# Performance work log

Hardware: AMD Instinct MI355X
Metric: run time of the kernel (lower is better)

Reference implementation:

```python
import jax, jax.numpy as jnp
from jax import lax
import numpy as np

B, N, C = 4, 2000, 80           # images, proposals/img, foreground classes
SCORE_THR = 0.05
IOU_THR = 0.5
MAX_PER_IMG = 100
K_PRE = 2000                     # pre-NMS top-k candidates per image
STDS = np.array([0.1, 0.1, 0.2, 0.2], dtype=np.float32)
MAX_RATIO = float(abs(np.log(16.0 / 1000.0)))  # wh_ratio_clip=16/1000


def setup_inputs() -> dict:
    key = jax.random.key(0)
    k1, k2, k3 = jax.random.split(key, 3)
    class_outs = jax.random.normal(k1, (B, N, C + 1), dtype=jnp.float32)
    regression_outs = jax.random.normal(k2, (B, N, C * 4), dtype=jnp.float32) * 0.5
    # random valid proposal boxes inside 800x1333 images (x1<x2, y1<y2)
    xy = jax.random.uniform(k3, (B, N, 2, 2), dtype=jnp.float32)
    xy = xy * jnp.array([1333.0, 800.0], dtype=jnp.float32)
    lo = jnp.min(xy, axis=2)
    hi = jnp.max(xy, axis=2) + 1.0
    boxes = jnp.concatenate([lo, hi], axis=-1)  # [B,N,4] x1,y1,x2,y2
    images_hw = jnp.tile(jnp.array([[800, 1333]], dtype=jnp.int32), (B, 1))
    return {"class_outs": class_outs, "regression_outs": regression_outs,
            "boxes": boxes, "images_hw": images_hw}


def _decode(props, deltas, h, w):
    # props [N,4], deltas [N,C,4] -> decoded boxes [N,C,4], clipped to image
    d = deltas * jnp.asarray(STDS)
    dx, dy, dw, dh = d[..., 0], d[..., 1], d[..., 2], d[..., 3]
    dw = jnp.clip(dw, -MAX_RATIO, MAX_RATIO)
    dh = jnp.clip(dh, -MAX_RATIO, MAX_RATIO)
    px = (props[:, None, 0] + props[:, None, 2]) * 0.5
    py = (props[:, None, 1] + props[:, None, 3]) * 0.5
    pw = props[:, None, 2] - props[:, None, 0]
    ph = props[:, None, 3] - props[:, None, 1]
    gx = px + pw * dx
    gy = py + ph * dy
    gw = pw * jnp.exp(dw)
    gh = ph * jnp.exp(dh)
    x1 = jnp.clip(gx - gw * 0.5, 0.0, w)
    y1 = jnp.clip(gy - gh * 0.5, 0.0, h)
    x2 = jnp.clip(gx + gw * 0.5, 0.0, w)
    y2 = jnp.clip(gy + gh * 0.5, 0.0, h)
    return jnp.stack([x1, y1, x2, y2], axis=-1)


def _pairwise_iou(b):
    # b [K,4] -> iou [K,K]
    area = (b[:, 2] - b[:, 0]) * (b[:, 3] - b[:, 1])
    lt = jnp.maximum(b[:, None, :2], b[None, :, :2])
    rb = jnp.minimum(b[:, None, 2:], b[None, :, 2:])
    wh = jnp.clip(rb - lt, 0.0)
    inter = wh[..., 0] * wh[..., 1]
    return inter / (area[:, None] + area[None, :] - inter + 1e-6)


def _process_image(cls_out, reg_out, props, hw):
    h = hw[0].astype(jnp.float32)
    w = hw[1].astype(jnp.float32)
    scores = jax.nn.softmax(cls_out, axis=-1)[:, :C]          # drop background col
    bboxes = _decode(props, reg_out.reshape(N, C, 4), h, w)   # [N,C,4]
    flat_scores = scores.reshape(-1)                          # [N*C]
    flat_boxes = bboxes.reshape(-1, 4)
    labels = jnp.tile(jnp.arange(C, dtype=jnp.int32), N)      # class fastest-varying
    cand = jnp.where(flat_scores > SCORE_THR, flat_scores, -1.0)
    top_scores, top_idx = lax.top_k(cand, K_PRE)
    top_boxes = flat_boxes[top_idx]
    top_labels = labels[top_idx]
    valid = top_scores > SCORE_THR
    # class-offset trick: boxes of distinct classes never overlap
    off = top_labels.astype(jnp.float32)[:, None] * (jnp.maximum(h, w) + 1.0)
    iou = _pairwise_iou(top_boxes + off)                      # [K_PRE,K_PRE]
    idxs = jnp.arange(K_PRE)

    def body(i, keep):
        sup = (idxs > i) & (iou[i] > IOU_THR) & keep[i]
        return keep & ~sup

    keep = lax.fori_loop(0, K_PRE, body, valid)
    kept_scores = jnp.where(keep, top_scores, -1.0)
    det_scores, det_i = lax.top_k(kept_scores, MAX_PER_IMG)
    det_valid = det_scores > SCORE_THR
    det_boxes = jnp.where(det_valid[:, None], top_boxes[det_i], 0.0)
    det_labels = jnp.where(det_valid, top_labels[det_i], -1)
    det_scores = jnp.where(det_valid, det_scores, 0.0)
    return det_boxes, det_scores, det_labels


def reference(class_outs, regression_outs, boxes, images_hw):
    det_boxes, det_scores, det_labels = jax.vmap(_process_image)(
        class_outs, regression_outs, boxes, images_hw)
    return det_boxes, det_scores, det_labels
```

## Files before the change

kernel.cpp:

```cpp
#include <hip/hip_runtime.h>


typedef unsigned long long u64;
typedef unsigned int u32;

#define B_ 4
#define N_ 2000
#define C_ 80
#define NCLS 81
#define KPRE 2000
#define MAXDET 100
#define TARGET 256
#define NB 2312
#define NBPAD 2368
#define NG 37
#define HBASE 0xF500
#define KSHIFT 46
#define CAPA 320
#define CAPB 2048
#define NWAVE 16
#define SEGW 384
#define CAPBLK 128
#define BPI 125
#define BIGI 0x7fffffff

__device__ __forceinline__ u64 pack_key(float score, unsigned fi) {
  return ((u64)__float_as_uint(score) << 32) | (u64)(0xFFFFFFFFu - fi);
}

__device__ __forceinline__ float wred_max(float v) {
  int t;
#define STEPM(ctrl)                                                          \
  t = __builtin_amdgcn_update_dpp(__float_as_int(v), __float_as_int(v),      \
                                  (ctrl), 0xF, 0xF, false);                  \
  v = fmaxf(v, __int_as_float(t));
  STEPM(0x111) STEPM(0x112) STEPM(0x114) STEPM(0x118) STEPM(0x142) STEPM(0x143)
#undef STEPM
  return __int_as_float(__builtin_amdgcn_readlane(__float_as_int(v), 63));
}
__device__ __forceinline__ float wred_sum(float v) {
  int t;
#define STEPS(ctrl)                                                          \
  t = __builtin_amdgcn_update_dpp(0, __float_as_int(v), (ctrl), 0xF, 0xF,    \
                                  false);                                    \
  v = v + __int_as_float(t);
  STEPS(0x111) STEPS(0x112) STEPS(0x114) STEPS(0x118) STEPS(0x142) STEPS(0x143)
#undef STEPS
  return __int_as_float(__builtin_amdgcn_readlane(__float_as_int(v), 63));
}

__device__ __forceinline__ int dpp_min8(int v) {
  int t;
  t = __builtin_amdgcn_update_dpp(BIGI, v, 0x104, 0xF, 0xF, false);
  v = min(v, t);
  t = __builtin_amdgcn_update_dpp(BIGI, v, 0x102, 0xF, 0xF, false);
  v = min(v, t);
  t = __builtin_amdgcn_update_dpp(BIGI, v, 0x101, 0xF, 0xF, false);
  v = min(v, t);
  return v;
}

__device__ __forceinline__ float4 decode_one(
    u64 kk, const float* __restrict__ reg, const float* __restrict__ props,
    int b, float h, float w, float offscale) {
  const float MAXR = 4.135166556742356f;
  unsigned fi = 0xFFFFFFFFu - (u32)kk;
  int n = (int)(fi / (unsigned)C_);
  int c = (int)(fi - (unsigned)n * (unsigned)C_);
  float4 p = ((const float4*)props)[b * N_ + n];
  const float* dl = reg + ((size_t)(b * N_ + n)) * (C_ * 4) + c * 4;
  float dx = dl[0] * 0.1f;
  float dy = dl[1] * 0.1f;
  float dw = fminf(fmaxf(dl[2] * 0.2f, -MAXR), MAXR);
  float dh = fminf(fmaxf(dl[3] * 0.2f, -MAXR), MAXR);
  float px = (p.x + p.z) * 0.5f, py = (p.y + p.w) * 0.5f;
  float pw = p.z - p.x, ph = p.w - p.y;
  float gx = px + pw * dx, gy = py + ph * dy;
  float gw = pw * expf(dw), gh = ph * expf(dh);
  float off = (float)c * offscale;
  return make_float4(fminf(fmaxf(gx - gw * 0.5f, 0.0f), w) + off,
                     fminf(fmaxf(gy - gh * 0.5f, 0.0f), h) + off,
                     fminf(fmaxf(gx + gw * 0.5f, 0.0f), w) + off,
                     fminf(fmaxf(gy + gh * 0.5f, 0.0f), h) + off);
}

__global__ __launch_bounds__(1024) void cand_kernel(
    const float* __restrict__ cls, u64* __restrict__ gkeys, int* __restrict__ gcnt) {
  __shared__ int s_wc[16], s_woff[16];
  const int tid = threadIdx.x;
  const int w = tid >> 6, lane = tid & 63;
  const int blk = blockIdx.x;
  const int b = blk / BPI;
  const int n = (blk % BPI) * 16 + w;
  const float* lg = cls + (size_t)(b * N_ + n) * NCLS;
  float x0 = lg[lane];
  float x1 = (lane < 17) ? lg[64 + lane] : -3.0e38f;
  float mx = wred_max(fmaxf(x0, x1));
  float e0 = expf(x0 - mx);
  float e1 = (lane < 17) ? expf(x1 - mx) : 0.0f;
  float sum = wred_sum(e0 + e1);
  float sc0 = e0 / sum, sc1 = e1 / sum;
  bool p0 = sc0 > 0.05f;
  bool p1 = (lane < 16) && (sc1 > 0.05f);
  u64 m0 = __ballot(p0), m1 = __ballot(p1);
  int c0 = __popcll(m0);
  if (lane == 0) s_wc[w] = c0 + __popcll(m1);
  __syncthreads();
  if (tid == 0) {
    int acc = 0;
#pragma unroll
    for (int i = 0; i < 16; ++i) { s_woff[i] = acc; acc += s_wc[i]; }
    gcnt[blk] = acc;
  }
  __syncthreads();
  const int base = s_woff[w];
  const u64 lt = (1ull << lane) - 1;
  u64* gk = gkeys + (size_t)blk * CAPBLK;
  if (p0) {
    int slot = base + __popcll(m0 & lt);
    if (slot < CAPBLK) gk[slot] = pack_key(sc0, (unsigned)(n * C_ + lane));
  }
  if (p1) {
    int slot = base + c0 + __popcll(m1 & lt);
    if (slot < CAPBLK) gk[slot] = pack_key(sc1, (unsigned)(n * C_ + 64 + lane));
  }
}


__global__ __launch_bounds__(1024) void nms_kernel(
    const float* __restrict__ reg, const float* __restrict__ props,
    const int* __restrict__ hw, const u64* __restrict__ gkeys,
    const int* __restrict__ gcnt, float* __restrict__ out) {
  __shared__ u64 lds8[7952];
  char* bp = (char*)lds8;
  u64* keylist = (u64*)bp;
  u64* SS = (u64*)bp;
  u64* rb = (u64*)(bp + 8192);
  u64* U2 = (u64*)bp;
  u64* SSB = (u64*)(bp + 16384);
  u32* hist = (u32*)(bp + 49152);
  float4* bxA = (float4*)(bp + 49152);
  u64* U = (u64*)(bp + 58624);
  int* outl = (int*)(bp + 62720);
  int* misc = (int*)(bp + 63232);
  int* segc = (int*)(bp + 63296);
  int* s_coarse = (int*)(bp + 63360);

  const int b = blockIdx.x, tid = threadIdx.x;
  const int wv = tid >> 6, lane = tid & 63;

  float h = (float)hw[b * 2 + 0];
  float w = (float)hw[b * 2 + 1];
  float offscale = fmaxf(h, w) + 1.0f;

  if (tid < 16) misc[tid] = 0;
  if (tid < 64) s_coarse[tid] = 0;
  for (int i = tid; i < NBPAD; i += 1024) hist[i] = 0;
  __syncthreads();

  {
    int cnts[8];
#pragma unroll
    for (int k = 0; k < 8; k++) {
      int p = wv + 16 * k;
      cnts[k] = (p < BPI) ? gcnt[b * BPI + p] : 0;
    }
    bool ovf = false;
    int segoff = 0;
#pragma unroll
    for (int k = 0; k < 8; k++) {
      int p = wv + 16 * k;
      if (p >= BPI) break;
      int cnt = cnts[k];
      if (cnt > CAPBLK) { ovf = true; cnt = CAPBLK; }
      const u64* seg = gkeys + (size_t)(b * BPI + p) * CAPBLK;
#pragma unroll
      for (int r = 0; r < 2; r++) {
        int idx = lane + 64 * r;
        if (idx < cnt) {
          u64 key = seg[idx];
          int bi = min(max((int)(key >> KSHIFT) - HBASE, 0), NB - 1);
          atomicAdd(&hist[bi], 1u);
          int slot = segoff + idx;
          if (slot < SEGW) keylist[wv * SEGW + slot] = key;
        }
      }
      segoff += cnt;
    }
    if (segoff > SEGW) ovf = true;
    if (lane == 0) {
      segc[wv] = min(segoff, SEGW);
      if (ovf) misc[7] = 1;
    }
  }
  __syncthreads();

  for (int g2 = wv; g2 < NG; g2 += NWAVE) {
    int v = (int)hist[(g2 << 6) | lane];
#pragma unroll
    for (int o = 32; o; o >>= 1) v += __shfl_xor(v, o);
    if (lane == 0) s_coarse[g2] = v;
  }
  __syncthreads();

  if (tid < 64) {
    int v = s_coarse[lane];
#pragma unroll
    for (int off = 1; off < 64; off <<= 1) {
      int src = lane + off;
      int o = __shfl(v, src < 64 ? src : 63);
      if (src < 64) v += o;
    }
    int Mtot = __shfl(v, 0);
    u64 pm = __ballot(v >= TARGET);
    int T_A = 0, S_A;
    if (pm) {
      int gs = 63 - __builtin_clzll(pm);
      int beyond = __shfl(v, gs + 1);
      int fv = (int)hist[(gs << 6) | lane];
#pragma unroll
      for (int off = 1; off < 64; off <<= 1) {
        int src = lane + off;
        int o = __shfl(fv, src < 64 ? src : 63);
        if (src < 64) fv += o;
      }
      int cum = beyond + fv;
      u64 pm2 = __ballot(cum >= TARGET);
      int tr = 63 - __builtin_clzll(pm2);
      T_A = (gs << 6) + tr;
      S_A = __shfl(cum, tr);
    } else {
      S_A = Mtot;
    }
    u64 pmB = __ballot(v >= KPRE);
    int T_B = 0, S_B;
    if (pmB) {
      int gs = 63 - __builtin_clzll(pmB);
      int beyond = __shfl(v, gs + 1);
      int fv = (int)hist[(gs << 6) | lane];
#pragma unroll
      for (int off = 1; off < 64; off <<= 1) {
        int src = lane + off;
        int o = __shfl(fv, src < 64 ? src : 63);
        if (src < 64) fv += o;
      }
      int cum = beyond + fv;
      u64 pm2 = __ballot(cum >= KPRE);
      int tr = 63 - __builtin_clzll(pm2);
      T_B = (gs << 6) + tr;
      S_B = __shfl(cum, tr);
    } else {
      S_B = Mtot;
    }
    if (lane == 0) {
      misc[0] = T_A; misc[2] = S_A; misc[3] = Mtot;
      misc[1] = T_B; misc[8] = S_B; misc[4] = 0;
    }
  }
  __syncthreads();
  if (tid == 0 && misc[8] > CAPB)
    misc[1] = min(misc[1] + 1, NB - 1);
  __syncthreads();

  int T_A = misc[0], S_A = misc[2], Mtot = misc[3];
  bool modeB = (S_A > CAPA) || (misc[7] != 0);
  int K = 0, nkept = 0;

  if (!modeB) {
    for (int s = 0; s < NWAVE; s++) {
      int Mg = segc[s];
      bool pred = false;
      u64 key = 0;
      if (tid < Mg) {
        key = keylist[s * SEGW + tid];
        int bi = min(max((int)(key >> KSHIFT) - HBASE, 0), NB - 1);
        pred = (bi >= T_A);
      }
      u64 mk = __ballot(pred);
      if (mk) {
        int wbase = 0;
        if (lane == 0) wbase = atomicAdd(&misc[4], __popcll(mk));
        wbase = __shfl(wbase, 0);
        if (pred) {
          int pos = wbase + __popcll(mk & ((1ull << lane) - 1));
          if (pos < CAPA) U[pos] = key;
        }
      }
    }
    __syncthreads();
    int S = misc[4];
    if (S > CAPA) S = CAPA;
    if (tid == 0 && (S & 1)) U[S] = 0ULL;
    __syncthreads();
    if (tid < S) {
      u64 k1 = U[tid];
      int r1 = 0;
      const ulonglong2* Uu2 = (const ulonglong2*)U;
      int half = (S + 1) >> 1;
      for (int k = 0; k < half; k++) {
        ulonglong2 kk = Uu2[k];
        r1 += (kk.x > k1) + (kk.y > k1);
      }
      SS[r1] = k1;
    }
    __syncthreads();
    K = S;
    for (int j = tid; j < K; j += 1024)
      bxA[j] = decode_one(SS[j], reg, props, b, h, w, offscale);
    __syncthreads();

    int nwords = (S + 63) >> 6;
    int ntiles = nwords * (nwords + 1) / 2;
    for (int t = wv; t < ntiles; t += NWAVE) {
      int ti = 0, rem = t;
      while (rem >= nwords - ti) { rem -= nwords - ti; ti++; }
      int tj = ti + rem;
      int i = (ti << 6) + lane;
      float4 bi4 = bxA[i];
      float ai = (bi4.z - bi4.x) * (bi4.w - bi4.y);
      u64 bits = 0;
      int jbase = tj << 6;
      int jcount = min(64, S - jbase);
      for (int jj = 0; jj < jcount; jj++) {
        int j = jbase + jj;
        float4 bj = bxA[j];
        float aj = (bj.z - bj.x) * (bj.w - bj.y);
        float iw = fmaxf(fminf(bi4.z, bj.z) - fmaxf(bi4.x, bj.x), 0.0f);
        float ih = fmaxf(fminf(bi4.w, bj.w) - fmaxf(bi4.y, bj.y), 0.0f);
        float inter = iw * ih;
        float iou = inter / (ai + aj - inter + 1e-6f);
        if (j > i && iou > 0.5f) bits |= (1ull << jj);
      }
      if (i < S) rb[i * 8 + tj] = bits;
    }
    __syncthreads();

    if (tid < 64) {
      u64 alive = 0;
      if (lane < nwords) {
        alive = ~0ull;
        int remb = S & 63;
        if (lane == nwords - 1 && remb) alive = (1ull << remb) - 1;
      }
      int nk = 0;
      if (S > 0) {
        int i = 0;
        u64 row = (lane < nwords) ? rb[0 * 8 + lane] : 0ull;
        for (;;) {
          if (lane == 0) outl[nk] = i;
          nk++;
          if (nk >= MAXDET) break;
          if (lane == (i >> 6)) alive &= ~(1ull << (i & 63));
          u64 rowSpec = (i + 1 < S && lane < nwords) ? rb[(i + 1) * 8 + lane] : 0ull;
          u64 a2 = alive & ~row;
          alive = a2;
          int cnd = a2 ? ((lane << 6) + (int)__builtin_ctzll(a2)) : BIGI;
          int m8 = dpp_min8(cnd);
          int ni = __builtin_amdgcn_readfirstlane(m8);
          if (ni >= BIGI) break;
          row = (ni == i + 1) ? rowSpec
                              : ((lane < nwords) ? rb[ni * 8 + lane] : 0ull);
          i = ni;
        }
      }
      if (lane == 0) misc[6] = nk;
    }
    __syncthreads();
    nkept = misc[6];
    if (nkept < MAXDET && K < Mtot && K < KPRE) modeB = true;
  }

  if (modeB) {
    __syncthreads();
    if (tid == 0) misc[4] = 0;
    __syncthreads();
    int T_B = misc[1];
    for (int k = 0; k < 8; k++) {
      int p = wv + 16 * k;
      if (p >= BPI) break;
      int cnt = min(gcnt[b * BPI + p], CAPBLK);
      const u64* seg = gkeys + (size_t)(b * BPI + p) * CAPBLK;
#pragma unroll
      for (int r = 0; r < 2; r++) {
        int idx = lane + 64 * r;
        bool pred = false;
        u64 key = 0;
        if (idx < cnt) {
          key = seg[idx];
          int bi = min(max((int)(key >> KSHIFT) - HBASE, 0), NB - 1);
          pred = (bi >= T_B);
        }
        u64 mk = __ballot(pred);
        if (mk) {
          int wbase = 0;
          if (lane == 0) wbase = atomicAdd(&misc[4], __popcll(mk));
          wbase = __shfl(wbase, 0);
          if (pred) {
            int pos = wbase + __popcll(mk & ((1ull << lane) - 1));
            if (pos < CAPB) U2[pos] = key;
          }
        }
      }
    }
    __syncthreads();
    int S = misc[4];
    if (S > CAPB) S = CAPB;
    {
      int j1 = tid, j2 = tid + 1024;
      u64 k1 = (j1 < S) ? U2[j1] : 0ULL;
      u64 k2 = (j2 < S) ? U2[j2] : 0ULL;
      int r1 = 0, r2 = 0;
      for (int k = 0; k < S; k++) {
        u64 kk = U2[k];
        r1 += (kk > k1);
        r2 += (kk > k2);
      }
      __syncthreads();
      if (j1 < S) SSB[r1] = k1;
      if (j2 < S) SSB[r2] = k2;
    }
    __syncthreads();
    K = (S < KPRE) ? S : KPRE;
    int j1 = tid, j2 = tid + 1024;
    bool kp1 = (j1 < K), kp2 = (j2 < K);
    float4 bb1 = kp1 ? decode_one(SSB[j1], reg, props, b, h, w, offscale)
                     : make_float4(0, 0, 0, 0);
    float4 bb2 = kp2 ? decode_one(SSB[j2], reg, props, b, h, w, offscale)
                     : make_float4(0, 0, 0, 0);
    int nk = 0;
    if (K > 0) {
      int i = 0;
      for (;;) {
        if (tid == 0) { outl[nk] = i; misc[5] = K; }
        nk++;
        if (nk >= MAXDET) break;
        __syncthreads();
        float4 tb = decode_one(SSB[i], reg, props, b, h, w, offscale);
        float ai = (tb.z - tb.x) * (tb.w - tb.y);
        int ln = K;
        if (kp1 && j1 > i) {
          float aj = (bb1.z - bb1.x) * (bb1.w - bb1.y);
          float iw = fmaxf(fminf(tb.z, bb1.z) - fmaxf(tb.x, bb1.x), 0.0f);
          float ih = fmaxf(fminf(tb.w, bb1.w) - fmaxf(tb.y, bb1.y), 0.0f);
          float inter = iw * ih;
          float iou = inter / (ai + aj - inter + 1e-6f);
          if (iou > 0.5f) kp1 = false;
          else ln = min(ln, j1);
        }
        if (kp2 && j2 > i) {
          float aj = (bb2.z - bb2.x) * (bb2.w - bb2.y);
          float iw = fmaxf(fminf(tb.z, bb2.z) - fmaxf(tb.x, bb2.x), 0.0f);
          float ih = fmaxf(fminf(tb.w, bb2.w) - fmaxf(tb.y, bb2.y), 0.0f);
          float inter = iw * ih;
          float iou = inter / (ai + aj - inter + 1e-6f);
          if (iou > 0.5f) kp2 = false;
          else ln = min(ln, j2);
        }
#pragma unroll
        for (int off = 32; off; off >>= 1) ln = min(ln, __shfl_xor(ln, off));
        if ((tid & 63) == 0 && ln < K) atomicMin(&misc[5], ln);
        __syncthreads();
        int ni = misc[5];
        __syncthreads();
        if (ni >= K) break;
        i = ni;
      }
    }
    if (tid == 0) misc[6] = nk;
    __syncthreads();
    nkept = misc[6];
  }

  float* oBox = out;
  float* oSc = out + B_ * MAXDET * 4;
  float* oLb = out + B_ * MAXDET * 5;
  for (int k2 = tid; k2 < MAXDET; k2 += 1024) {
    float4 bb = make_float4(0.0f, 0.0f, 0.0f, 0.0f);
    float sv = 0.0f, lv = -1.0f;
    if (k2 < nkept) {
      int idx = outl[k2];
      u64 kk = modeB ? SSB[idx] : SS[idx];
      sv = __uint_as_float((u32)(kk >> 32));
      unsigned fi = 0xFFFFFFFFu - (u32)kk;
      int c = (int)(fi % (unsigned)C_);
      float off = (float)c * offscale;
      float4 ob = modeB ? decode_one(kk, reg, props, b, h, w, offscale) : bxA[idx];
      bb = make_float4(ob.x - off, ob.y - off, ob.z - off, ob.w - off);
      lv = (float)c;
    }
    oBox[(b * MAXDET + k2) * 4 + 0] = bb.x;
    oBox[(b * MAXDET + k2) * 4 + 1] = bb.y;
    oBox[(b * MAXDET + k2) * 4 + 2] = bb.z;
    oBox[(b * MAXDET + k2) * 4 + 3] = bb.w;
    oSc[b * MAXDET + k2] = sv;
    oLb[b * MAXDET + k2] = lv;
  }
}

extern "C" void kernel_launch(void* const* d_in, const int* in_sizes, int n_in,
                              void* d_out, int out_size, void* d_ws, size_t ws_size,
                              hipStream_t stream) {
  const float* cls = (const float*)d_in[0];
  const float* reg = (const float*)d_in[1];
  const float* props = (const float*)d_in[2];
  const int* hw = (const int*)d_in[3];
  float* out = (float*)d_out;

  int* gcnt = (int*)d_ws;
  u64* gkeys = (u64*)((char*)d_ws + 2048);

  cand_kernel<<<B_ * BPI, 1024, 0, stream>>>(cls, gkeys, gcnt);
  nms_kernel<<<B_, 1024, 0, stream>>>(reg, props, hw, gkeys, gcnt, out);
}
```

Baseline: 108.0 us.

## Split NMS kernel into fast-path and fallback kernels gated by flag

Splits the single NMS kernel into a fast-path kernel (mode A) and a separate fallback kernel (mode B), which early-exits unless a per-image global flag says the fast path was insufficient. The fallback recomputes its own histogram threshold instead of sharing one from the fast path. The intent is to shrink register and code pressure in the common path and drop the T_B computation from it. It adds an extra kernel launch and an extra pass over the keys when the fallback does run.

Measured after the change: 107.2 us. Within noise of the previous version (-0.7%).

```diff
diff --git a/kernel.cpp b/kernel.cpp
--- a/kernel.cpp
+++ b/kernel.cpp
@@ -126,18 +126,16 @@
   }
 }
 
-
-__global__ __launch_bounds__(1024) void nms_kernel(
+__global__ __launch_bounds__(1024) void nmsA_kernel(
     const float* __restrict__ reg, const float* __restrict__ props,
     const int* __restrict__ hw, const u64* __restrict__ gkeys,
-    const int* __restrict__ gcnt, float* __restrict__ out) {
+    const int* __restrict__ gcnt, int* __restrict__ gflag,
+    float* __restrict__ out) {
   __shared__ u64 lds8[7952];
   char* bp = (char*)lds8;
   u64* keylist = (u64*)bp;
   u64* SS = (u64*)bp;
   u64* rb = (u64*)(bp + 8192);
-  u64* U2 = (u64*)bp;
-  u64* SSB = (u64*)(bp + 16384);
   u32* hist = (u32*)(bp + 49152);
   float4* bxA = (float4*)(bp + 49152);
   u64* U = (u64*)(bp + 58624);
@@ -232,34 +230,8 @@
     } else {
       S_A = Mtot;
     }
-    u64 pmB = __ballot(v >= KPRE);
-    int T_B = 0, S_B;
-    if (pmB) {
-      int gs = 63 - __builtin_clzll(pmB);
-      int beyond = __shfl(v, gs + 1);
-      int fv = (int)hist[(gs << 6) | lane];
-#pragma unroll
-      for (int off = 1; off < 64; off <<= 1) {
-        int src = lane + off;
-        int o = __shfl(fv, src < 64 ? src : 63);
-        if (src < 64) fv += o;
-      }
-      int cum = beyond + fv;
-      u64 pm2 = __ballot(cum >= KPRE);
-      int tr = 63 - __builtin_clzll(pm2);
-      T_B = (gs << 6) + tr;
-      S_B = __shfl(cum, tr);
-    } else {
-      S_B = Mtot;
-    }
-    if (lane == 0) {
-      misc[0] = T_A; misc[2] = S_A; misc[3] = Mtot;
-      misc[1] = T_B; misc[8] = S_B; misc[4] = 0;
-    }
-  }
-  __syncthreads();
-  if (tid == 0 && misc[8] > CAPB)
-    misc[1] = min(misc[1] + 1, NB - 1);
+    if (lane == 0) { misc[0] = T_A; misc[2] = S_A; misc[3] = Mtot; misc[4] = 0; }
+  }
   __syncthreads();
 
   int T_A = misc[0], S_A = misc[2], Mtot = misc[3];
@@ -370,106 +342,8 @@
     if (nkept < MAXDET && K < Mtot && K < KPRE) modeB = true;
   }
 
-  if (modeB) {
-    __syncthreads();
-    if (tid == 0) misc[4] = 0;
-    __syncthreads();
-    int T_B = misc[1];
-    for (int k = 0; k < 8; k++) {
-      int p = wv + 16 * k;
-      if (p >= BPI) break;
-      int cnt = min(gcnt[b * BPI + p], CAPBLK);
-      const u64* seg = gkeys + (size_t)(b * BPI + p) * CAPBLK;
-#pragma unroll
-      for (int r = 0; r < 2; r++) {
-        int idx = lane + 64 * r;
-        bool pred = false;
-        u64 key = 0;
-        if (idx < cnt) {
-          key = seg[idx];
-          int bi = min(max((int)(key >> KSHIFT) - HBASE, 0), NB - 1);
-          pred = (bi >= T_B);
-        }
-        u64 mk = __ballot(pred);
-        if (mk) {
-          int wbase = 0;
-          if (lane == 0) wbase = atomicAdd(&misc[4], __popcll(mk));
-          wbase = __shfl(wbase, 0);
-          if (pred) {
-            int pos = wbase + __popcll(mk & ((1ull << lane) - 1));
-            if (pos < CAPB) U2[pos] = key;
-          }
-        }
-      }
-    }
-    __syncthreads();
-    int S = misc[4];
-    if (S > CAPB) S = CAPB;
-    {
-      int j1 = tid, j2 = tid + 1024;
-      u64 k1 = (j1 < S) ? U2[j1] : 0ULL;
-      u64 k2 = (j2 < S) ? U2[j2] : 0ULL;
-      int r1 = 0, r2 = 0;
-      for (int k = 0; k < S; k++) {
-        u64 kk = U2[k];
-        r1 += (kk > k1);
-        r2 += (kk > k2);
-      }
-      __syncthreads();
-      if (j1 < S) SSB[r1] = k1;
-      if (j2 < S) SSB[r2] = k2;
-    }
-    __syncthreads();
-    K = (S < KPRE) ? S : KPRE;
-    int j1 = tid, j2 = tid + 1024;
-    bool kp1 = (j1 < K), kp2 = (j2 < K);
-    float4 bb1 = kp1 ? decode_one(SSB[j1], reg, props, b, h, w, offscale)
-                     : make_float4(0, 0, 0, 0);
-    float4 bb2 = kp2 ? decode_one(SSB[j2], reg, props, b, h, w, offscale)
-                     : make_float4(0, 0, 0, 0);
-    int nk = 0;
-    if (K > 0) {
-      int i = 0;
-      for (;;) {
-        if (tid == 0) { outl[nk] = i; misc[5] = K; }
-        nk++;
-        if (nk >= MAXDET) break;
-        __syncthreads();
-        float4 tb = decode_one(SSB[i], reg, props, b, h, w, offscale);
-        float ai = (tb.z - tb.x) * (tb.w - tb.y);
-        int ln = K;
-        if (kp1 && j1 > i) {
-          float aj = (bb1.z - bb1.x) * (bb1.w - bb1.y);
-          float iw = fmaxf(fminf(tb.z, bb1.z) - fmaxf(tb.x, bb1.x), 0.0f);
-          float ih = fmaxf(fminf(tb.w, bb1.w) - fmaxf(tb.y, bb1.y), 0.0f);
-          float inter = iw * ih;
-          float iou = inter / (ai + aj - inter + 1e-6f);
-          if (iou > 0.5f) kp1 = false;
-          else ln = min(ln, j1);
-        }
-        if (kp2 && j2 > i) {
-          float aj = (bb2.z - bb2.x) * (bb2.w - bb2.y);
-          float iw = fmaxf(fminf(tb.z, bb2.z) - fmaxf(tb.x, bb2.x), 0.0f);
-          float ih = fmaxf(fminf(tb.w, bb2.w) - fmaxf(tb.y, bb2.y), 0.0f);
-          float inter = iw * ih;
-          float iou = inter / (ai + aj - inter + 1e-6f);
-          if (iou > 0.5f) kp2 = false;
-          else ln = min(ln, j2);
-        }
-#pragma unroll
-        for (int off = 32; off; off >>= 1) ln = min(ln, __shfl_xor(ln, off));
-        if ((tid & 63) == 0 && ln < K) atomicMin(&misc[5], ln);
-        __syncthreads();
-        int ni = misc[5];
-        __syncthreads();
-        if (ni >= K) break;
-        i = ni;
-      }
-    }
-    if (tid == 0) misc[6] = nk;
-    __syncthreads();
-    nkept = misc[6];
-  }
+  if (tid == 0) gflag[b] = modeB ? 1 : 0;
+  if (modeB) return;
 
   float* oBox = out;
   float* oSc = out + B_ * MAXDET * 4;
@@ -479,12 +353,188 @@
     float sv = 0.0f, lv = -1.0f;
     if (k2 < nkept) {
       int idx = outl[k2];
-      u64 kk = modeB ? SSB[idx] : SS[idx];
+      u64 kk = SS[idx];
       sv = __uint_as_float((u32)(kk >> 32));
       unsigned fi = 0xFFFFFFFFu - (u32)kk;
       int c = (int)(fi % (unsigned)C_);
       float off = (float)c * offscale;
-      float4 ob = modeB ? decode_one(kk, reg, props, b, h, w, offscale) : bxA[idx];
+      float4 ob = bxA[idx];
+      bb = make_float4(ob.x - off, ob.y - off, ob.z - off, ob.w - off);
+      lv = (float)c;
+    }
+    oBox[(b * MAXDET + k2) * 4 + 0] = bb.x;
+    oBox[(b * MAXDET + k2) * 4 + 1] = bb.y;
+    oBox[(b * MAXDET + k2) * 4 + 2] = bb.z;
+    oBox[(b * MAXDET + k2) * 4 + 3] = bb.w;
+    oSc[b * MAXDET + k2] = sv;
+    oLb[b * MAXDET + k2] = lv;
+  }
+}
+
+__global__ __launch_bounds__(1024) void nmsB_kernel(
+    const float* __restrict__ reg, const float* __restrict__ props,
+    const int* __restrict__ hw, const u64* __restrict__ gkeys,
+    const int* __restrict__ gcnt, const int* __restrict__ gflag,
+    float* __restrict__ out) {
+  const int b = blockIdx.x, tid = threadIdx.x;
+  if (gflag[b] == 0) return;
+
+  __shared__ u64 lds8[7952];
+  char* bp = (char*)lds8;
+  u32* hist = (u32*)(bp + 0);
+  u64* U2 = (u64*)(bp + 9472);
+  u64* SSB = (u64*)(bp + 25856);
+  int* outl = (int*)(bp + 42240);
+  int* misc = (int*)(bp + 42752);
+  const int wv = tid >> 6, lane = tid & 63;
+
+  float h = (float)hw[b * 2 + 0];
+  float w = (float)hw[b * 2 + 1];
+  float offscale = fmaxf(h, w) + 1.0f;
+
+  for (int i = tid; i < NBPAD; i += 1024) hist[i] = 0;
+  if (tid < 16) misc[tid] = 0;
+  __syncthreads();
+
+  for (int k = 0; k < 8; k++) {
+    int p = wv + 16 * k;
+    if (p >= BPI) break;
+    int cnt = min(gcnt[b * BPI + p], CAPBLK);
+    const u64* seg = gkeys + (size_t)(b * BPI + p) * CAPBLK;
+#pragma unroll
+    for (int r = 0; r < 2; r++) {
+      int idx = lane + 64 * r;
+      if (idx < cnt) {
+        u64 key = seg[idx];
+        int bi = min(max((int)(key >> KSHIFT) - HBASE, 0), NB - 1);
+        atomicAdd(&hist[bi], 1u);
+      }
+    }
+  }
+  __syncthreads();
+
+  if (tid == 0) {
+    int acc = 0, tb = 0;
+    for (int bi = NB - 1; bi >= 0; bi--) {
+      acc += (int)hist[bi];
+      if (acc >= KPRE) { tb = bi; break; }
+    }
+    if (acc > CAPB) tb = min(tb + 1, NB - 1);
+    misc[1] = tb;
+    misc[4] = 0;
+  }
+  __syncthreads();
+  int T_B = misc[1];
+
+  for (int k = 0; k < 8; k++) {
+    int p = wv + 16 * k;
+    if (p >= BPI) break;
+    int cnt = min(gcnt[b * BPI + p], CAPBLK);
+    const u64* seg = gkeys + (size_t)(b * BPI + p) * CAPBLK;
+#pragma unroll
+    for (int r = 0; r < 2; r++) {
+      int idx = lane + 64 * r;
+      bool pred = false;
+      u64 key = 0;
+      if (idx < cnt) {
+        key = seg[idx];
+        int bi = min(max((int)(key >> KSHIFT) - HBASE, 0), NB - 1);
+        pred = (bi >= T_B);
+      }
+      u64 mk = __ballot(pred);
+      if (mk) {
+        int wbase = 0;
+        if (lane == 0) wbase = atomicAdd(&misc[4], __popcll(mk));
+        wbase = __shfl(wbase, 0);
+        if (pred) {
+          int pos = wbase + __popcll(mk & ((1ull << lane) - 1));
+          if (pos < CAPB) U2[pos] = key;
+        }
+      }
+    }
+  }
+  __syncthreads();
+  int S = misc[4];
+  if (S > CAPB) S = CAPB;
+  {
+    int j1 = tid, j2 = tid + 1024;
+    u64 k1 = (j1 < S) ? U2[j1] : 0ULL;
+    u64 k2 = (j2 < S) ? U2[j2] : 0ULL;
+    int r1 = 0, r2 = 0;
+    for (int k = 0; k < S; k++) {
+      u64 kk = U2[k];
+      r1 += (kk > k1);
+      r2 += (kk > k2);
+    }
+    __syncthreads();
+    if (j1 < S) SSB[r1] = k1;
+    if (j2 < S) SSB[r2] = k2;
+  }
+  __syncthreads();
+  int K = (S < KPRE) ? S : KPRE;
+  int j1 = tid, j2 = tid + 1024;
+  bool kp1 = (j1 < K), kp2 = (j2 < K);
+  float4 bb1 = kp1 ? decode_one(SSB[j1], reg, props, b, h, w, offscale)
+                   : make_float4(0, 0, 0, 0);
+  float4 bb2 = kp2 ? decode_one(SSB[j2], reg, props, b, h, w, offscale)
+                   : make_float4(0, 0, 0, 0);
+  int nk = 0;
+  if (K > 0) {
+    int i = 0;
+    for (;;) {
+      if (tid == 0) { outl[nk] = i; misc[5] = K; }
+      nk++;
+      if (nk >= MAXDET) break;
+      __syncthreads();
+      float4 tb = decode_one(SSB[i], reg, props, b, h, w, offscale);
+      float ai = (tb.z - tb.x) * (tb.w - tb.y);
+      int ln = K;
+      if (kp1 && j1 > i) {
+        float aj = (bb1.z - bb1.x) * (bb1.w - bb1.y);
+        float iw = fmaxf(fminf(tb.z, bb1.z) - fmaxf(tb.x, bb1.x), 0.0f);
+        float ih = fmaxf(fminf(tb.w, bb1.w) - fmaxf(tb.y, bb1.y), 0.0f);
+        float inter = iw * ih;
+        float iou = inter / (ai + aj - inter + 1e-6f);
+        if (iou > 0.5f) kp1 = false;
+        else ln = min(ln, j1);
+      }
+      if (kp2 && j2 > i) {
+        float aj = (bb2.z - bb2.x) * (bb2.w - bb2.y);
+        float iw = fmaxf(fminf(tb.z, bb2.z) - fmaxf(tb.x, bb2.x), 0.0f);
+        float ih = fmaxf(fminf(tb.w, bb2.w) - fmaxf(tb.y, bb2.y), 0.0f);
+        float inter = iw * ih;
+        float iou = inter / (ai + aj - inter + 1e-6f);
+        if (iou > 0.5f) kp2 = false;
+        else ln = min(ln, j2);
+      }
+#pragma unroll
+      for (int off = 32; off; off >>= 1) ln = min(ln, __shfl_xor(ln, off));
+      if ((tid & 63) == 0 && ln < K) atomicMin(&misc[5], ln);
+      __syncthreads();
+      int ni = misc[5];
+      __syncthreads();
+      if (ni >= K) break;
+      i = ni;
+    }
+  }
+  if (tid == 0) misc[6] = nk;
+  __syncthreads();
+  int nkept = misc[6];
+
+  float* oBox = out;
+  float* oSc = out + B_ * MAXDET * 4;
+  float* oLb = out + B_ * MAXDET * 5;
+  for (int k2 = tid; k2 < MAXDET; k2 += 1024) {
+    float4 bb = make_float4(0.0f, 0.0f, 0.0f, 0.0f);
+    float sv = 0.0f, lv = -1.0f;
+    if (k2 < nkept) {
+      int idx = outl[k2];
+      u64 kk = SSB[idx];
+      sv = __uint_as_float((u32)(kk >> 32));
+      unsigned fi = 0xFFFFFFFFu - (u32)kk;
+      int c = (int)(fi % (unsigned)C_);
+      float off = (float)c * offscale;
+      float4 ob = decode_one(kk, reg, props, b, h, w, offscale);
       bb = make_float4(ob.x - off, ob.y - off, ob.z - off, ob.w - off);
       lv = (float)c;
     }
@@ -508,7 +558,9 @@
 
   int* gcnt = (int*)d_ws;
   u64* gkeys = (u64*)((char*)d_ws + 2048);
+  int* gflag = (int*)((char*)d_ws + 514048);
 
   cand_kernel<<<B_ * BPI, 1024, 0, stream>>>(cls, gkeys, gcnt);
-  nms_kernel<<<B_, 1024, 0, stream>>>(reg, props, hw, gkeys, gcnt, out);
-}
+  nmsA_kernel<<<B_, 1024, 0, stream>>>(reg, props, hw, gkeys, gcnt, gflag, out);
+  nmsB_kernel<<<B_, 1024, 0, stream>>>(reg, props, hw, gkeys, gcnt, gflag, out);
+}
```
